# Performance work log

Measured on AMD Instinct MI355X. Metric: run time of the kernel, lower is better.

## Reference

```python
import jax, jax.numpy as jnp
import numpy as np

BATCH, SEQ, H_IN, N_STATE, H_OUT = 16, 4096, 128, 256, 128
RMIN, RMAX, MAX_PHASE = 0.9, 1.0, 6.283


def setup_inputs() -> dict:
    key = jax.random.key(0)
    ks = jax.random.split(key, 9)
    u = jax.random.normal(ks[0], (BATCH, SEQ, H_IN), jnp.float32)
    # LRU exponential parameterization init (matches torch __init__)
    u1 = jax.random.uniform(ks[1], (N_STATE,), jnp.float32)
    u2 = jax.random.uniform(ks[2], (N_STATE,), jnp.float32)
    nu_log = jnp.log(-0.5 * jnp.log(u1 * (RMAX + RMIN) * (RMAX - RMIN) + RMIN ** 2))
    theta_log = jnp.log(MAX_PHASE * u2)
    lam_abs = jnp.exp(-jnp.exp(nu_log))
    gamma_log = jnp.log(jnp.sqrt(1.0 - lam_abs ** 2))
    s2in = np.sqrt(2.0 * H_IN).astype(np.float32)
    B_re = jax.random.normal(ks[3], (N_STATE, H_IN), jnp.float32) / s2in
    B_im = jax.random.normal(ks[4], (N_STATE, H_IN), jnp.float32) / s2in
    sst = np.sqrt(float(N_STATE)).astype(np.float32)
    C_re = jax.random.normal(ks[5], (H_OUT, N_STATE), jnp.float32) / sst
    C_im = jax.random.normal(ks[6], (H_OUT, N_STATE), jnp.float32) / sst
    D = jax.random.normal(ks[7], (H_OUT, H_IN), jnp.float32) / np.sqrt(float(H_IN)).astype(np.float32)
    return dict(u=u, nu_log=nu_log, theta_log=theta_log, gamma_log=gamma_log,
                B_re=B_re, B_im=B_im, C_re=C_re, C_im=C_im, D=D)


def _combine(a, b):
    # complex affine composition: (l, x) o (l', x') -> (l*l', l'*x + x')
    l1r, l1i, x1r, x1i = a
    l2r, l2i, x2r, x2i = b
    lr = l1r * l2r - l1i * l2i
    li = l1r * l2i + l1i * l2r
    xr = l2r * x1r - l2i * x1i + x2r
    xi = l2r * x1i + l2i * x1r + x2i
    return (lr, li, xr, xi)


def reference(u, nu_log, theta_log, gamma_log, B_re, B_im, C_re, C_im, D):
    lam_mod = jnp.exp(-jnp.exp(nu_log))          # |lambda|, [N]
    th = jnp.exp(theta_log)
    lam_re = lam_mod * jnp.cos(th)
    lam_im = lam_mod * jnp.sin(th)
    gammas = jnp.exp(gamma_log)                  # [N]
    # input projection Bu_t = gamma * (B @ u_t), complex -> real/imag parts
    Bu_re = jnp.einsum('blh,nh->bln', u, B_re) * gammas  # [B,L,N]
    Bu_im = jnp.einsum('blh,nh->bln', u, B_im) * gammas
    Bsz, L, N = Bu_re.shape
    lr = jnp.broadcast_to(lam_re, (Bsz, L, N))
    li = jnp.broadcast_to(lam_im, (Bsz, L, N))
    # parallel scan of x_t = lambda * x_{t-1} + Bu_t, x0 = 0
    _, _, xr, xi = jax.lax.associative_scan(_combine, (lr, li, Bu_re, Bu_im), axis=1)
    zero = jnp.zeros((Bsz, 1, N), u.dtype)
    pre_re = jnp.concatenate([zero, xr[:, :-1]], axis=1)  # states[:, :-1]
    pre_im = jnp.concatenate([zero, xi[:, :-1]], axis=1)
    # y_t = Re(C x_{t-1}) + D u_t
    y = (jnp.einsum('bln,on->blo', pre_re, C_re)
         - jnp.einsum('bln,on->blo', pre_im, C_im)
         + jnp.einsum('blh,oh->blo', u, D))
    return y
```

## Files before the change

kernel.cpp:

```cpp
#include <hip/hip_runtime.h>
#include <math.h>

#define BATCH 16
#define SEQ   4096
#define HIN   128
#define NST   256
#define HOUT  128
#define CL    32
#define NC    (SEQ/CL)
#define ROWS  (BATCH*SEQ)
#define KTOT  640
#define NPRE  512

typedef __attribute__((ext_vector_type(8))) short short8;
typedef __attribute__((ext_vector_type(4))) float f32x4;

__device__ inline unsigned short f2bf(float f) {
  union { float f; unsigned u; } v; v.f = f;
  unsigned r = v.u + 0x7FFFu + ((v.u >> 16) & 1u);
  return (unsigned short)(r >> 16);
}
__device__ inline float bf2f(unsigned short s) {
  union { unsigned u; float f; } v; v.u = ((unsigned)s) << 16;
  return v.f;
}
__device__ inline float bits2f(unsigned u) {
  union { unsigned u; float f; } v; v.u = u; return v.f;
}

__global__ __launch_bounds__(256) void k_prep(
    const float* __restrict__ nu_log, const float* __restrict__ theta_log,
    const float* __restrict__ gamma_log,
    const float* __restrict__ Bre, const float* __restrict__ Bim,
    const float* __restrict__ Cre, const float* __restrict__ Cim,
    const float* __restrict__ Dm,
    float* __restrict__ lamre, float* __restrict__ lamim,
    unsigned* __restrict__ lamPk,
    unsigned short* __restrict__ Wb, unsigned short* __restrict__ W) {
  int idx = blockIdx.x*256 + threadIdx.x;
  if (idx < NST) {
    float lm = expf(-expf(nu_log[idx]));
    float th = expf(theta_log[idx]);
    float lr = lm * cosf(th), li = lm * sinf(th);
    lamre[idx] = lr; lamim[idx] = li;
    float pr = 1.f, pi = 0.f;
    for (int j = 0; j < CL; ++j) {
      lamPk[j*NST + idx] = ((unsigned)f2bf(pi) << 16) | (unsigned)f2bf(pr);
      float nr = pr*lr - pi*li;
      float ni = pr*li + pi*lr;
      pr = nr; pi = ni;
    }
  }
  if (idx < 512*HIN) {
    int r = idx >> 7, h = idx & 127;
    int g = r >> 7;
    int w = r & 127;
    int n = g*64 + (w & 63);
    float gm = expf(gamma_log[n]);
    float v = (w < 64) ? Bre[n*HIN + h] : Bim[n*HIN + h];
    Wb[idx] = f2bf(gm * v);
  }
  if (idx < HOUT*KTOT) {
    int o = idx / KTOT, k = idx - o*KTOT;
    float v;
    if (k < NST)        v =  Cre[o*NST + k];
    else if (k < 2*NST) v = -Cim[o*NST + (k - NST)];
    else                v =  Dm[o*HIN + (k - 2*NST)];
    W[idx] = f2bf(v);
  }
}

union SharedBu {
  unsigned short B[128][136];
  unsigned short stgb[4][32][132];
};
__global__ __launch_bounds__(256) void k_bu(
    const float* __restrict__ u, const unsigned short* __restrict__ Wb,
    const float* __restrict__ lamre, const float* __restrict__ lamim,
    unsigned short* __restrict__ preL,
    float* __restrict__ S_re, float* __restrict__ S_im) {
  __shared__ unsigned short Asl[128][136];
  __shared__ SharedBu sh;
  int tid = threadIdx.x;
  int row0 = blockIdx.x * 128;
  int wid = tid >> 6, lane = tid & 63;
  int lm = lane & 15, lq = lane >> 4;
  int m0 = (wid >> 1) * 64, n0 = (wid & 1) * 64;
  int b = row0 >> 12;
  int cbase = (row0 & 4095) >> 5;
#pragma unroll
  for (int cc = 0; cc < 8; ++cc) {
    int ch = cc*256 + tid;
    int r = ch >> 4, h0 = (ch & 15) * 8;
    const float* src = u + (size_t)(row0 + r)*HIN + h0;
    float4 v0 = *(const float4*)src;
    float4 v1 = *(const float4*)(src + 4);
    unsigned short o[8];
    o[0]=f2bf(v0.x); o[1]=f2bf(v0.y); o[2]=f2bf(v0.z); o[3]=f2bf(v0.w);
    o[4]=f2bf(v1.x); o[5]=f2bf(v1.y); o[6]=f2bf(v1.z); o[7]=f2bf(v1.w);
    *(short8*)&Asl[r][h0] = *(const short8*)o;
  }
  for (int g = 0; g < 4; ++g) {
    __syncthreads();
#pragma unroll
    for (int cc = 0; cc < 8; ++cc) {
      int ch = cc*256 + tid;
      int r = ch >> 4, h0 = (ch & 15) * 8;
      *(short8*)&sh.B[r][h0] = *(const short8*)&Wb[(size_t)(g*128 + r)*HIN + h0];
    }
    __syncthreads();
    f32x4 acc[4][4];
#pragma unroll
    for (int i = 0; i < 4; ++i)
#pragma unroll
      for (int j = 0; j < 4; ++j) acc[i][j] = (f32x4)0.f;
#pragma unroll
    for (int ks = 0; ks < 4; ++ks) {
      int k0 = ks*32 + lq*8;
      short8 a[4], bb[4];
#pragma unroll
      for (int i = 0; i < 4; ++i) a[i] = *(const short8*)&Asl[m0 + i*16 + lm][k0];
#pragma unroll
      for (int j = 0; j < 4; ++j) bb[j] = *(const short8*)&sh.B[n0 + j*16 + lm][k0];
#pragma unroll
      for (int i = 0; i < 4; ++i)
#pragma unroll
        for (int j = 0; j < 4; ++j)
          acc[i][j] = __builtin_amdgcn_mfma_f32_16x16x32_bf16(a[i], bb[j], acc[i][j], 0, 0, 0);
    }
    __syncthreads();
#pragma unroll
    for (int i = 0; i < 4; ++i)
#pragma unroll
      for (int j = 0; j < 4; ++j)
#pragma unroll
        for (int r = 0; r < 4; ++r) {
          int row = m0 + i*16 + lq*4 + r;
          sh.stgb[row >> 5][row & 31][n0 + j*16 + lm] = f2bf(acc[i][j][r]);
        }
    __syncthreads();
    {
      int ck = tid >> 6, nl = tid & 63;
      int ng = g*64 + nl;
      float lr = lamre[ng], li = lamim[ng];
      float rr[CL], ri[CL];
#pragma unroll
      for (int t = 0; t < CL; ++t) {
        rr[t] = bf2f(sh.stgb[ck][t][nl]);
        ri[t] = bf2f(sh.stgb[ck][t][64 + nl]);
      }
      int rowb = row0 + ck*32;
      unsigned short* pl = preL + (size_t)rowb*NPRE;
      float sr = 0.f, si = 0.f;
#pragma unroll
      for (int t = 0; t < CL; ++t) {
        pl[ng]       = f2bf(sr);
        pl[NST + ng] = f2bf(si);
        float nr = lr*sr - li*si + rr[t];
        float ni = lr*si + li*sr + ri[t];
        sr = nr; si = ni; pl += NPRE;
      }
      int c = cbase + ck;
      int idx = (b*NC + c)*NST + ng;
      S_re[idx] = sr; S_im[idx] = si;
    }
  }
}

__global__ __launch_bounds__(64) void k_scan(
    const float* __restrict__ S_re, const float* __restrict__ S_im,
    const float* __restrict__ lamre, const float* __restrict__ lamim,
    unsigned* __restrict__ X0Pk) {
  int b = blockIdx.x >> 2;
  int n = (blockIdx.x & 3) * 64 + threadIdx.x;
  float ar = lamre[n], ai = lamim[n];
#pragma unroll
  for (int s = 0; s < 5; ++s) { float nr = ar*ar - ai*ai, ni = 2.f*ar*ai; ar = nr; ai = ni; }
  const float* Sr = S_re + (size_t)b*NC*NST + n;
  const float* Si = S_im + (size_t)b*NC*NST + n;
  unsigned* Xp = X0Pk + (size_t)b*NC*NST + n;
  float Are[16], Aim[16], Bre[16], Bim[16];
#pragma unroll
  for (int cc = 0; cc < 16; ++cc) { Are[cc] = Sr[cc*NST]; Aim[cc] = Si[cc*NST]; }
  float xr = 0.f, xi = 0.f;
#pragma unroll
  for (int seg = 0; seg < 8; ++seg) {
    if (seg < 7) {
      const float* pr = Sr + (size_t)(seg+1)*16*NST;
      const float* pi = Si + (size_t)(seg+1)*16*NST;
      if (seg & 1) {
#pragma unroll
        for (int cc = 0; cc < 16; ++cc) { Are[cc] = pr[cc*NST]; Aim[cc] = pi[cc*NST]; }
      } else {
#pragma unroll
        for (int cc = 0; cc < 16; ++cc) { Bre[cc] = pr[cc*NST]; Bim[cc] = pi[cc*NST]; }
      }
    }
#pragma unroll
    for (int cc = 0; cc < 16; ++cc) {
      Xp[(size_t)(seg*16 + cc)*NST] = ((unsigned)f2bf(xi) << 16) | (unsigned)f2bf(xr);
      float cr = (seg & 1) ? Bre[cc] : Are[cc];
      float ci = (seg & 1) ? Bim[cc] : Aim[cc];
      float nr = ar*xr - ai*xi + cr;
      float ni = ar*xi + ai*xr + ci;
      xr = nr; xi = ni;
    }
  }
}

__global__ __launch_bounds__(256) void k_out2(
    const unsigned short* __restrict__ preL, const float* __restrict__ u,
    const unsigned short* __restrict__ W,
    const unsigned* __restrict__ lamPk, const unsigned* __restrict__ X0Pk,
    float* __restrict__ y) {
  __shared__ unsigned short Asl[128][136];
  __shared__ unsigned short Bsl[128][136];
  int tid = threadIdx.x;
  int row0 = blockIdx.x * 128;
  int wid = tid >> 6, lane = tid & 63;
  int lm = lane & 15, lq = lane >> 4;
  int m0 = wid * 32;
  f32x4 acc[2][8];
#pragma unroll
  for (int i = 0; i < 2; ++i)
#pragma unroll
    for (int j = 0; j < 8; ++j) acc[i][j] = (f32x4)0.f;
  for (int s = 0; s < 5; ++s) {
    __syncthreads();
#pragma unroll
    for (int cc = 0; cc < 8; ++cc) {
      int ch = cc*256 + tid;
      int r = ch >> 4, h0 = (ch & 15) * 8;
      *(short8*)&Bsl[r][h0] = *(const short8*)&W[(size_t)r*KTOT + s*128 + h0];
    }
    if (s < 4) {
#pragma unroll
      for (int cc = 0; cc < 8; ++cc) {
        int ch = cc*256 + tid;
        int r = ch >> 4, h0 = (ch & 15) * 8;
        int grow = row0 + r;
        int j32 = r & 31;
        int cidx = grow >> 5;
        int n = ((s & 1) << 7) + h0;
        short8 loc = *(const short8*)&preL[(size_t)grow*NPRE + s*128 + h0];
        uint4 lp0 = *(const uint4*)&lamPk[j32*NST + n];
        uint4 lp1 = *(const uint4*)&lamPk[j32*NST + n + 4];
        uint4 xp0 = *(const uint4*)&X0Pk[(size_t)cidx*NST + n];
        uint4 xp1 = *(const uint4*)&X0Pk[(size_t)cidx*NST + n + 4];
        unsigned lps[8] = {lp0.x, lp0.y, lp0.z, lp0.w, lp1.x, lp1.y, lp1.z, lp1.w};
        unsigned xps[8] = {xp0.x, xp0.y, xp0.z, xp0.w, xp1.x, xp1.y, xp1.z, xp1.w};
        unsigned short o[8];
#pragma unroll
        for (int e = 0; e < 8; ++e) {
          float lr = bits2f(lps[e] << 16);
          float li = bits2f(lps[e] & 0xFFFF0000u);
          float xr = bits2f(xps[e] << 16);
          float xi = bits2f(xps[e] & 0xFFFF0000u);
          float lv = bf2f((unsigned short)loc[e]);
          float v = (s < 2) ? (lv + lr*xr - li*xi)
                            : (lv + lr*xi + li*xr);
          o[e] = f2bf(v);
        }
        *(short8*)&Asl[r][h0] = *(const short8*)o;
      }
    } else {
#pragma unroll
      for (int cc = 0; cc < 8; ++cc) {
        int ch = cc*256 + tid;
        int r = ch >> 4, h0 = (ch & 15) * 8;
        const float* src = u + (size_t)(row0 + r)*HIN + h0;
        float4 v0 = *(const float4*)src;
        float4 v1 = *(const float4*)(src + 4);
        unsigned short o[8];
        o[0]=f2bf(v0.x); o[1]=f2bf(v0.y); o[2]=f2bf(v0.z); o[3]=f2bf(v0.w);
        o[4]=f2bf(v1.x); o[5]=f2bf(v1.y); o[6]=f2bf(v1.z); o[7]=f2bf(v1.w);
        *(short8*)&Asl[r][h0] = *(const short8*)o;
      }
    }
    __syncthreads();
#pragma unroll
    for (int ks = 0; ks < 4; ++ks) {
      int k0 = ks*32 + lq*8;
      short8 a[2], bb[8];
#pragma unroll
      for (int i = 0; i < 2; ++i) a[i] = *(const short8*)&Asl[m0 + i*16 + lm][k0];
#pragma unroll
      for (int j = 0; j < 8; ++j) bb[j] = *(const short8*)&Bsl[j*16 + lm][k0];
#pragma unroll
      for (int i = 0; i < 2; ++i)
#pragma unroll
        for (int j = 0; j < 8; ++j)
          acc[i][j] = __builtin_amdgcn_mfma_f32_16x16x32_bf16(a[i], bb[j], acc[i][j], 0, 0, 0);
    }
  }
#pragma unroll
  for (int i = 0; i < 2; ++i)
#pragma unroll
    for (int j = 0; j < 8; ++j)
#pragma unroll
      for (int r = 0; r < 4; ++r)
        y[(size_t)(row0 + m0 + i*16 + lq*4 + r)*HOUT + j*16 + lm] = acc[i][j][r];
}

extern "C" void kernel_launch(void* const* d_in, const int* in_sizes, int n_in,
                              void* d_out, int out_size, void* d_ws, size_t ws_size,
                              hipStream_t stream) {
  const float* u         = (const float*)d_in[0];
  const float* nu_log    = (const float*)d_in[1];
  const float* theta_log = (const float*)d_in[2];
  const float* gamma_log = (const float*)d_in[3];
  const float* B_re      = (const float*)d_in[4];
  const float* B_im      = (const float*)d_in[5];
  const float* C_re      = (const float*)d_in[6];
  const float* C_im      = (const float*)d_in[7];
  const float* Dm        = (const float*)d_in[8];
  float* y = (float*)d_out;
  char* ws = (char*)d_ws;

  size_t off = 0;
  float* lamre = (float*)(ws + off);            off += 1024;
  float* lamim = (float*)(ws + off);            off += 1024;
  unsigned* lamPk = (unsigned*)(ws + off);      off += 32768;
  unsigned short* Wb = (unsigned short*)(ws + off); off += 131072;
  unsigned short* W  = (unsigned short*)(ws + off); off += 163840;
  unsigned short* preL = (unsigned short*)(ws + off); off += (size_t)ROWS*NPRE*2;
  float* S_re = (float*)(ws + off);             off += 2097152;
  float* S_im = (float*)(ws + off);             off += 2097152;
  unsigned* X0Pk = (unsigned*)(ws + off);       off += 2097152;

  k_prep<<<320, 256, 0, stream>>>(nu_log, theta_log, gamma_log, B_re, B_im,
                                  C_re, C_im, Dm, lamre, lamim, lamPk, Wb, W);
  k_bu<<<ROWS/128, 256, 0, stream>>>(u, Wb, lamre, lamim, preL, S_re, S_im);
  k_scan<<<64, 64, 0, stream>>>(S_re, S_im, lamre, lamim, X0Pk);
  k_out2<<<ROWS/128, 256, 0, stream>>>(preL, u, W, lamPk, X0Pk, y);
}
```

Measured before the change: 165.7 us.

## Load weight fragments directly from global into registers, shrink LDS for occupancy

Both GEMM kernels stop staging the weight tile in LDS and instead have each lane load its MFMA B-fragments straight from global memory, double-buffered in registers across k-steps. k_bu also shrinks its chunk-scan staging buffer to two 32-row slices processed in two passes by half the threads. Launch bounds now request 3 blocks per SM. The aim is lower LDS use for higher occupancy and fewer barriers, at the cost of uncoalesced global/L2 weight reads, more register pressure, and a serialized scan phase on half the threads.

```diff
diff --git a/kernel.cpp b/kernel.cpp
--- a/kernel.cpp
+++ b/kernel.cpp
@@ -70,17 +70,13 @@
   }
 }
 
-union SharedBu {
-  unsigned short B[128][136];
-  unsigned short stgb[4][32][132];
-};
-__global__ __launch_bounds__(256) void k_bu(
+__global__ __launch_bounds__(256, 3) void k_bu(
     const float* __restrict__ u, const unsigned short* __restrict__ Wb,
     const float* __restrict__ lamre, const float* __restrict__ lamim,
     unsigned short* __restrict__ preL,
     float* __restrict__ S_re, float* __restrict__ S_im) {
   __shared__ unsigned short Asl[128][136];
-  __shared__ SharedBu sh;
+  __shared__ unsigned short stgb[2][32][132];
   int tid = threadIdx.x;
   int row0 = blockIdx.x * 128;
   int wid = tid >> 6, lane = tid & 63;
@@ -100,69 +96,75 @@
     o[4]=f2bf(v1.x); o[5]=f2bf(v1.y); o[6]=f2bf(v1.z); o[7]=f2bf(v1.w);
     *(short8*)&Asl[r][h0] = *(const short8*)o;
   }
+  __syncthreads();
   for (int g = 0; g < 4; ++g) {
-    __syncthreads();
-#pragma unroll
-    for (int cc = 0; cc < 8; ++cc) {
-      int ch = cc*256 + tid;
-      int r = ch >> 4, h0 = (ch & 15) * 8;
-      *(short8*)&sh.B[r][h0] = *(const short8*)&Wb[(size_t)(g*128 + r)*HIN + h0];
-    }
-    __syncthreads();
+    const unsigned short* WbG = Wb + (size_t)(g*128)*HIN;
     f32x4 acc[4][4];
 #pragma unroll
     for (int i = 0; i < 4; ++i)
 #pragma unroll
       for (int j = 0; j < 4; ++j) acc[i][j] = (f32x4)0.f;
+    short8 bb[2][4];
+#pragma unroll
+    for (int j = 0; j < 4; ++j)
+      bb[0][j] = *(const short8*)&WbG[(size_t)(n0 + j*16 + lm)*HIN + lq*8];
 #pragma unroll
     for (int ks = 0; ks < 4; ++ks) {
       int k0 = ks*32 + lq*8;
-      short8 a[4], bb[4];
+      if (ks < 3) {
+        int k1 = (ks+1)*32 + lq*8;
+#pragma unroll
+        for (int j = 0; j < 4; ++j)
+          bb[(ks+1)&1][j] = *(const short8*)&WbG[(size_t)(n0 + j*16 + lm)*HIN + k1];
+      }
+      short8 a[4];
 #pragma unroll
       for (int i = 0; i < 4; ++i) a[i] = *(const short8*)&Asl[m0 + i*16 + lm][k0];
 #pragma unroll
-      for (int j = 0; j < 4; ++j) bb[j] = *(const short8*)&sh.B[n0 + j*16 + lm][k0];
-#pragma unroll
       for (int i = 0; i < 4; ++i)
 #pragma unroll
         for (int j = 0; j < 4; ++j)
-          acc[i][j] = __builtin_amdgcn_mfma_f32_16x16x32_bf16(a[i], bb[j], acc[i][j], 0, 0, 0);
-    }
-    __syncthreads();
-#pragma unroll
-    for (int i = 0; i < 4; ++i)
-#pragma unroll
-      for (int j = 0; j < 4; ++j)
-#pragma unroll
-        for (int r = 0; r < 4; ++r) {
-          int row = m0 + i*16 + lq*4 + r;
-          sh.stgb[row >> 5][row & 31][n0 + j*16 + lm] = f2bf(acc[i][j][r]);
+          acc[i][j] = __builtin_amdgcn_mfma_f32_16x16x32_bf16(a[i], bb[ks&1][j], acc[i][j], 0, 0, 0);
+    }
+    for (int p = 0; p < 2; ++p) {
+      __syncthreads();
+#pragma unroll
+      for (int ii = 0; ii < 2; ++ii) {
+        int i = 2*p + ii;
+#pragma unroll
+        for (int j = 0; j < 4; ++j)
+#pragma unroll
+          for (int r = 0; r < 4; ++r) {
+            int trow = ii*16 + lq*4 + r;
+            stgb[wid >> 1][trow][n0 + j*16 + lm] = f2bf(acc[i][j][r]);
+          }
+      }
+      __syncthreads();
+      if (tid < 128) {
+        int buf = tid >> 6, nl = tid & 63;
+        int ng = g*64 + nl;
+        float lr = lamre[ng], li = lamim[ng];
+        float rr[CL], ri[CL];
+#pragma unroll
+        for (int t = 0; t < CL; ++t) {
+          rr[t] = bf2f(stgb[buf][t][nl]);
+          ri[t] = bf2f(stgb[buf][t][64 + nl]);
         }
-    __syncthreads();
-    {
-      int ck = tid >> 6, nl = tid & 63;
-      int ng = g*64 + nl;
-      float lr = lamre[ng], li = lamim[ng];
-      float rr[CL], ri[CL];
-#pragma unroll
-      for (int t = 0; t < CL; ++t) {
-        rr[t] = bf2f(sh.stgb[ck][t][nl]);
-        ri[t] = bf2f(sh.stgb[ck][t][64 + nl]);
-      }
-      int rowb = row0 + ck*32;
-      unsigned short* pl = preL + (size_t)rowb*NPRE;
-      float sr = 0.f, si = 0.f;
-#pragma unroll
-      for (int t = 0; t < CL; ++t) {
-        pl[ng]       = f2bf(sr);
-        pl[NST + ng] = f2bf(si);
-        float nr = lr*sr - li*si + rr[t];
-        float ni = lr*si + li*sr + ri[t];
-        sr = nr; si = ni; pl += NPRE;
-      }
-      int c = cbase + ck;
-      int idx = (b*NC + c)*NST + ng;
-      S_re[idx] = sr; S_im[idx] = si;
+        int rowb = row0 + buf*64 + p*32;
+        unsigned short* pl = preL + (size_t)rowb*NPRE;
+        float sr = 0.f, si = 0.f;
+#pragma unroll
+        for (int t = 0; t < CL; ++t) {
+          pl[ng]       = f2bf(sr);
+          pl[NST + ng] = f2bf(si);
+          float nr = lr*sr - li*si + rr[t];
+          float ni = lr*si + li*sr + ri[t];
+          sr = nr; si = ni; pl += NPRE;
+        }
+        int c = cbase + buf*2 + p;
+        int idx = (b*NC + c)*NST + ng;
+        S_re[idx] = sr; S_im[idx] = si;
+      }
     }
   }
 }
@@ -208,13 +210,12 @@
   }
 }
 
-__global__ __launch_bounds__(256) void k_out2(
+__global__ __launch_bounds__(256, 3) void k_out2(
     const unsigned short* __restrict__ preL, const float* __restrict__ u,
     const unsigned short* __restrict__ W,
     const unsigned* __restrict__ lamPk, const unsigned* __restrict__ X0Pk,
     float* __restrict__ y) {
   __shared__ unsigned short Asl[128][136];
-  __shared__ unsigned short Bsl[128][136];
   int tid = threadIdx.x;
   int row0 = blockIdx.x * 128;
   int wid = tid >> 6, lane = tid & 63;
@@ -227,12 +228,10 @@
     for (int j = 0; j < 8; ++j) acc[i][j] = (f32x4)0.f;
   for (int s = 0; s < 5; ++s) {
     __syncthreads();
-#pragma unroll
-    for (int cc = 0; cc < 8; ++cc) {
-      int ch = cc*256 + tid;
-      int r = ch >> 4, h0 = (ch & 15) * 8;
-      *(short8*)&Bsl[r][h0] = *(const short8*)&W[(size_t)r*KTOT + s*128 + h0];
-    }
+    short8 bw[2][8];
+#pragma unroll
+    for (int j = 0; j < 8; ++j)
+      bw[0][j] = *(const short8*)&W[(size_t)(j*16 + lm)*KTOT + s*128 + lq*8];
     if (s < 4) {
 #pragma unroll
       for (int cc = 0; cc < 8; ++cc) {
@@ -281,16 +280,20 @@
 #pragma unroll
     for (int ks = 0; ks < 4; ++ks) {
       int k0 = ks*32 + lq*8;
-      short8 a[2], bb[8];
+      if (ks < 3) {
+        int k1 = (ks+1)*32 + lq*8;
+#pragma unroll
+        for (int j = 0; j < 8; ++j)
+          bw[(ks+1)&1][j] = *(const short8*)&W[(size_t)(j*16 + lm)*KTOT + s*128 + k1];
+      }
+      short8 a[2];
 #pragma unroll
       for (int i = 0; i < 2; ++i) a[i] = *(const short8*)&Asl[m0 + i*16 + lm][k0];
 #pragma unroll
-      for (int j = 0; j < 8; ++j) bb[j] = *(const short8*)&Bsl[j*16 + lm][k0];
-#pragma unroll
       for (int i = 0; i < 2; ++i)
 #pragma unroll
         for (int j = 0; j < 8; ++j)
-          acc[i][j] = __builtin_amdgcn_mfma_f32_16x16x32_bf16(a[i], bb[j], acc[i][j], 0, 0, 0);
+          acc[i][j] = __builtin_amdgcn_mfma_f32_16x16x32_bf16(a[i], bw[ks&1][j], acc[i][j], 0, 0, 0);
     }
   }
 #pragma unroll
```

New measurement: 209.4 us. 26.4% more time.

## Stage chunk-local scan outputs in LDS for coalesced 16-byte preL stores

Applied to the files above, without the earlier changes.

The within-chunk recurrence in k_bu used to write each bf16 state straight to global memory as scattered 2-byte stores, one row per step. It now writes the states back into the shared staging buffer, then copies whole rows to preL as 16-byte vectors. Because the staging buffer is halved, the epilogue runs in two passes with extra barriers, and only 128 threads do the serial scan in each pass. The goal is to cut uncoalesced global write traffic, at the cost of lower scan parallelism and more synchronisation.

```diff
diff --git a/kernel.cpp b/kernel.cpp
--- a/kernel.cpp
+++ b/kernel.cpp
@@ -72,7 +72,7 @@
 
 union SharedBu {
   unsigned short B[128][136];
-  unsigned short stgb[4][32][132];
+  unsigned short stgb[2][32][136];
 };
 __global__ __launch_bounds__(256) void k_bu(
     const float* __restrict__ u, const unsigned short* __restrict__ Wb,
@@ -128,41 +128,57 @@
         for (int j = 0; j < 4; ++j)
           acc[i][j] = __builtin_amdgcn_mfma_f32_16x16x32_bf16(a[i], bb[j], acc[i][j], 0, 0, 0);
     }
-    __syncthreads();
-#pragma unroll
-    for (int i = 0; i < 4; ++i)
-#pragma unroll
-      for (int j = 0; j < 4; ++j)
-#pragma unroll
-        for (int r = 0; r < 4; ++r) {
-          int row = m0 + i*16 + lq*4 + r;
-          sh.stgb[row >> 5][row & 31][n0 + j*16 + lm] = f2bf(acc[i][j][r]);
+    for (int p = 0; p < 2; ++p) {
+      __syncthreads();
+#pragma unroll
+      for (int ii = 0; ii < 2; ++ii) {
+        int i = 2*p + ii;
+#pragma unroll
+        for (int j = 0; j < 4; ++j)
+#pragma unroll
+          for (int r = 0; r < 4; ++r) {
+            int trow = ii*16 + lq*4 + r;
+            sh.stgb[wid >> 1][trow][n0 + j*16 + lm] = f2bf(acc[i][j][r]);
+          }
+      }
+      __syncthreads();
+      if (tid < 128) {
+        int buf = tid >> 6, nl = tid & 63;
+        int ng = g*64 + nl;
+        float lr = lamre[ng], li = lamim[ng];
+        float rr[CL], ri[CL];
+#pragma unroll
+        for (int t = 0; t < CL; ++t) {
+          rr[t] = bf2f(sh.stgb[buf][t][nl]);
+          ri[t] = bf2f(sh.stgb[buf][t][64 + nl]);
         }
-    __syncthreads();
-    {
-      int ck = tid >> 6, nl = tid & 63;
-      int ng = g*64 + nl;
-      float lr = lamre[ng], li = lamim[ng];
-      float rr[CL], ri[CL];
-#pragma unroll
-      for (int t = 0; t < CL; ++t) {
-        rr[t] = bf2f(sh.stgb[ck][t][nl]);
-        ri[t] = bf2f(sh.stgb[ck][t][64 + nl]);
-      }
-      int rowb = row0 + ck*32;
-      unsigned short* pl = preL + (size_t)rowb*NPRE;
-      float sr = 0.f, si = 0.f;
-#pragma unroll
-      for (int t = 0; t < CL; ++t) {
-        pl[ng]       = f2bf(sr);
-        pl[NST + ng] = f2bf(si);
-        float nr = lr*sr - li*si + rr[t];
-        float ni = lr*si + li*sr + ri[t];
-        sr = nr; si = ni; pl += NPRE;
-      }
-      int c = cbase + ck;
-      int idx = (b*NC + c)*NST + ng;
-      S_re[idx] = sr; S_im[idx] = si;
+        float sr = 0.f, si = 0.f;
+#pragma unroll
+        for (int t = 0; t < CL; ++t) {
+          sh.stgb[buf][t][nl]      = f2bf(sr);
+          sh.stgb[buf][t][64 + nl] = f2bf(si);
+          float nr = lr*sr - li*si + rr[t];
+          float ni = lr*si + li*sr + ri[t];
+          sr = nr; si = ni;
+        }
+        int c = cbase + buf*2 + p;
+        int idx = (b*NC + c)*NST + ng;
+        S_re[idx] = sr; S_im[idx] = si;
+      }
+      __syncthreads();
+#pragma unroll
+      for (int q = 0; q < 4; ++q) {
+        int uidx = q*256 + tid;
+        int buf = uidx >> 9;
+        int rem = uidx & 511;
+        int t   = rem >> 4;
+        int seg = rem & 15;
+        int im  = seg >> 3;
+        int c0  = (seg & 7)*8 + im*64;
+        int row = row0 + buf*64 + p*32 + t;
+        int dcol = im*256 + g*64 + (seg & 7)*8;
+        *(short8*)&preL[(size_t)row*NPRE + dcol] = *(const short8*)&sh.stgb[buf][t][c0];
+      }
     }
   }
 }
```

Measured after the change: 162.4 us. 2.0% less time.
